# Performance work log

Measured on AMD Instinct MI355X. Metric: run time of the kernel, lower is better.

## Reference

```python
import jax, jax.numpy as jnp
import numpy as np

M, N, D, P = 16, 4096, 128, 8192
H = N // D


def setup_inputs() -> dict:
    key = jax.random.key(0)
    ks = jax.random.split(key, 6)
    return {
        "X": jax.random.normal(ks[0], (M, N), dtype=jnp.float32),
        "W_q": jax.random.normal(ks[1], (N, N), dtype=jnp.float32) / np.sqrt(N),
        "W_k": jax.random.normal(ks[2], (N, N), dtype=jnp.float32) / np.sqrt(N),
        "W_v": jax.random.normal(ks[3], (N, N), dtype=jnp.float32) / np.sqrt(N),
        "cache_K": jax.random.normal(ks[4], (H, P, D), dtype=jnp.float32),
        "cache_V": jax.random.normal(ks[5], (H, P, D), dtype=jnp.float32),
    }


def _rms(x):
    # unaffine RMS norm over last dim, no eps (matches torch source)
    return x * jax.lax.rsqrt(jnp.mean(jnp.square(x), axis=-1, keepdims=True))


def reference(X, W_q, W_k, W_v, cache_K, cache_V):
    m, n = X.shape
    h, p, d = cache_K.shape
    # QKV projections -> [H, M, D]
    q = (X @ W_q).reshape(m, h, d).swapaxes(0, 1)
    k = (X @ W_k).reshape(m, h, d).swapaxes(0, 1)
    v = (X @ W_v).reshape(m, h, d).swapaxes(0, 1)
    q_norm = _rms(q)
    k_norm = _rms(k)
    # prepend KV cache: [H, P+M, D]
    k_cache = jnp.concatenate([cache_K[:, :p, :], k_norm], axis=1)
    v_cache = jnp.concatenate([cache_V[:, :p, :], v], axis=1)
    # attention WITHOUT 1/sqrt(D) scaling (matches torch source)
    scores = jnp.einsum("hmd,hpd->hmp", q_norm, k_cache)
    weights = jax.nn.softmax(scores, axis=-1)
    out = jnp.einsum("hmp,hpd->hmd", weights, v_cache)  # [H, M, D]
    return out.swapaxes(0, 1).reshape(m, n)
```

## Files before the change

kernel.cpp:

```cpp
#include <hip/hip_runtime.h>
#include <math.h>

#define M_ 16
#define N_ 4096
#define D_ 128
#define P_ 8192
#define H_ 32

#define NIC 32
#define ICH (N_/NIC)
#define NCB 16

#define CHUNK 128
#define NCH (P_/CHUNK)
#define NCH1 (NCH+1)

#define QKV_SZ    (3*H_*M_*D_)
#define PART_OFF  (QKV_SZ)
#define OPART_OFF (QKV_SZ)
#define OPART_SZ  (H_*NCH1*M_*D_)
#define ML_OFF    (OPART_OFF + OPART_SZ)

__global__ __launch_bounds__(256) void k_proj(const float* __restrict__ X,
                                              const float* __restrict__ Wq,
                                              const float* __restrict__ Wk,
                                              const float* __restrict__ Wv,
                                              float* __restrict__ part) {
  const int mat = blockIdx.z;
  const float* __restrict__ W = (mat == 0) ? Wq : ((mat == 1) ? Wk : Wv);
  const int cb = blockIdx.x, ic = blockIdx.y;
  const int t = threadIdx.x;
  const int j0 = cb * 256 + t;
  const int i0 = ic * ICH;

  __shared__ __align__(16) float XT[ICH][20];

  {
    const int i_l = t & 127, mh = t >> 7;
#pragma unroll
    for (int r = 0; r < 8; ++r)
      XT[i_l][mh * 8 + r] = X[(size_t)(mh * 8 + r) * N_ + i0 + i_l];
  }
  __syncthreads();

  float acc[16];
#pragma unroll
  for (int m = 0; m < 16; ++m) acc[m] = 0.f;

#pragma unroll 8
  for (int i = 0; i < ICH; ++i) {
    const float wv = __builtin_nontemporal_load(W + (size_t)(i0 + i) * N_ + j0);
    float xr[16];
    {
      float4 xv;
      xv = *reinterpret_cast<const float4*>(&XT[i][0]);
      xr[0] = xv.x; xr[1] = xv.y; xr[2] = xv.z; xr[3] = xv.w;
      xv = *reinterpret_cast<const float4*>(&XT[i][4]);
      xr[4] = xv.x; xr[5] = xv.y; xr[6] = xv.z; xr[7] = xv.w;
      xv = *reinterpret_cast<const float4*>(&XT[i][8]);
      xr[8] = xv.x; xr[9] = xv.y; xr[10] = xv.z; xr[11] = xv.w;
      xv = *reinterpret_cast<const float4*>(&XT[i][12]);
      xr[12] = xv.x; xr[13] = xv.y; xr[14] = xv.z; xr[15] = xv.w;
    }
#pragma unroll
    for (int m = 0; m < 16; ++m) acc[m] = fmaf(xr[m], wv, acc[m]);
  }

#pragma unroll
  for (int m = 0; m < 16; ++m)
    __builtin_nontemporal_store(acc[m], part + (size_t)((mat * NIC + ic) * M_ + m) * N_ + j0);
}

__global__ __launch_bounds__(256) void k_reduce(const float* __restrict__ part,
                                                float* __restrict__ qkv) {
  const int mat = blockIdx.z, m = blockIdx.y, nc = blockIdx.x;
  const int t = threadIdx.x;
  const int n = nc * 256 + t;

  float s = 0.f;
#pragma unroll
  for (int ic = 0; ic < NIC; ++ic)
    s += __builtin_nontemporal_load(part + (size_t)((mat * NIC + ic) * M_ + m) * N_ + n);

  float ss = s * s;
#pragma unroll
  for (int off = 1; off < 64; off <<= 1) ss += __shfl_xor(ss, off);
  __shared__ float wsum[4];
  const int wave = t >> 6, lane = t & 63;
  if (lane == 0) wsum[wave] = ss;
  __syncthreads();
  const int half = t >> 7;
  const float tot = wsum[half * 2] + wsum[half * 2 + 1];
  const float scale = (mat < 2) ? rsqrtf(tot * (1.0f / 128.0f)) : 1.0f;

  const int h = n >> 7, d = n & 127;
  qkv[(size_t)((mat * H_ + h) * M_ + m) * D_ + d] = s * scale;
}

__device__ __forceinline__ float fold8(float a[8], int dq) {
#pragma unroll
  for (int i = 0; i < 4; ++i) {
    const float send = (dq & 4) ? a[i] : a[i + 4];
    const float recv = __shfl_xor(send, 4);
    a[i] = ((dq & 4) ? a[i + 4] : a[i]) + recv;
  }
#pragma unroll
  for (int i = 0; i < 2; ++i) {
    const float send = (dq & 2) ? a[i] : a[i + 2];
    const float recv = __shfl_xor(send, 2);
    a[i] = ((dq & 2) ? a[i + 2] : a[i]) + recv;
  }
  {
    const float send = (dq & 1) ? a[0] : a[1];
    const float recv = __shfl_xor(send, 1);
    a[0] = ((dq & 1) ? a[1] : a[0]) + recv;
  }
  return a[0];
}

__device__ __forceinline__ float dot16(const float* __restrict__ qrow,
                                       const float4 k0, const float4 k1,
                                       const float4 k2, const float4 k3) {
  const float4 q0 = *reinterpret_cast<const float4*>(qrow);
  const float4 q1 = *reinterpret_cast<const float4*>(qrow + 32);
  const float4 q2 = *reinterpret_cast<const float4*>(qrow + 64);
  const float4 q3 = *reinterpret_cast<const float4*>(qrow + 96);
  float s;
  s = q0.x * k0.x;
  s = fmaf(q0.y, k0.y, s); s = fmaf(q0.z, k0.z, s); s = fmaf(q0.w, k0.w, s);
  s = fmaf(q1.x, k1.x, s); s = fmaf(q1.y, k1.y, s);
  s = fmaf(q1.z, k1.z, s); s = fmaf(q1.w, k1.w, s);
  s = fmaf(q2.x, k2.x, s); s = fmaf(q2.y, k2.y, s);
  s = fmaf(q2.z, k2.z, s); s = fmaf(q2.w, k2.w, s);
  s = fmaf(q3.x, k3.x, s); s = fmaf(q3.y, k3.y, s);
  s = fmaf(q3.z, k3.z, s); s = fmaf(q3.w, k3.w, s);
  return s;
}

__global__ __launch_bounds__(512, 2) void k_attn(const float* __restrict__ cacheK,
                                                 const float* __restrict__ cacheV,
                                                 const float* __restrict__ qkv,
                                                 float* __restrict__ opart,
                                                 float* __restrict__ ml) {
  const int c = blockIdx.x, h = blockIdx.y;
  const int t = threadIdx.x;
  const int wave = t >> 6, lane = t & 63;
  const int valid = (c < NCH) ? CHUNK : M_;
  const float* __restrict__ Ksrc = (c < NCH)
      ? (cacheK + ((size_t)h * P_ + (size_t)c * CHUNK) * D_)
      : (qkv + (size_t)((1 * H_ + h) * M_) * D_);
  const float* __restrict__ Vsrc = (c < NCH)
      ? (cacheV + ((size_t)h * P_ + (size_t)c * CHUNK) * D_)
      : (qkv + (size_t)((2 * H_ + h) * M_) * D_);

  __shared__ __align__(16) float smem[8192];
  __shared__ __align__(16) float mlx[8][8][2];

  float* qs = smem;
  float* wxp = smem + 2048 + wave * 128;

  {
    const float4* src = reinterpret_cast<const float4*>(qkv + (size_t)(h * M_) * D_);
    reinterpret_cast<float4*>(qs)[t] = src[t];
  }
  __syncthreads();

  const int pg = lane >> 3, dq = lane & 7;
  const int dl = lane * 2;
  const int rg = wave >> 1, mbase = (wave & 1) * 8;
  const int rbase = rg * 32;
  int rc = valid - rbase; rc = (rc < 0) ? 0 : ((rc > 32) ? 32 : rc);
  const int nb = rc >> 4;

  float mrun = -3.0e38f, lrun = 0.f;
  float2 o[8];
#pragma unroll
  for (int mi = 0; mi < 8; ++mi) o[mi] = make_float2(0.f, 0.f);

#pragma unroll 1
  for (int b = 0; b < nb; ++b) {
    const int r0 = rbase + b * 16;

    float4 kA0, kA1, kA2, kA3, kB0, kB1, kB2, kB3;
    {
      const float* ka = Ksrc + (size_t)(r0 + pg) * D_ + dq * 4;
      kA0 = *reinterpret_cast<const float4*>(ka);
      kA1 = *reinterpret_cast<const float4*>(ka + 32);
      kA2 = *reinterpret_cast<const float4*>(ka + 64);
      kA3 = *reinterpret_cast<const float4*>(ka + 96);
      const float* kb = Ksrc + (size_t)(r0 + 8 + pg) * D_ + dq * 4;
      kB0 = *reinterpret_cast<const float4*>(kb);
      kB1 = *reinterpret_cast<const float4*>(kb + 32);
      kB2 = *reinterpret_cast<const float4*>(kb + 64);
      kB3 = *reinterpret_cast<const float4*>(kb + 96);
    }

    float a[8];
#pragma unroll
    for (int mi = 0; mi < 8; ++mi) {
      a[mi] = dot16(qs + (mbase + mi) * D_ + dq * 4, kA0, kA1, kA2, kA3);
      __builtin_amdgcn_sched_barrier(0);
    }
    const float sA = fold8(a, dq);

#pragma unroll
    for (int mi = 0; mi < 8; ++mi) {
      a[mi] = dot16(qs + (mbase + mi) * D_ + dq * 4, kB0, kB1, kB2, kB3);
      __builtin_amdgcn_sched_barrier(0);
    }
    const float sB = fold8(a, dq);

    float tmax = fmaxf(sA, sB);
    tmax = fmaxf(tmax, __shfl_xor(tmax, 8));
    tmax = fmaxf(tmax, __shfl_xor(tmax, 16));
    tmax = fmaxf(tmax, __shfl_xor(tmax, 32));
    const float mnew = fmaxf(mrun, tmax);
    const float fc = __expf(mrun - mnew);
    mrun = mnew;
    const float wA = __expf(sA - mnew);
    const float wB = __expf(sB - mnew);
    float rs = wA + wB;
    rs += __shfl_xor(rs, 8); rs += __shfl_xor(rs, 16); rs += __shfl_xor(rs, 32);
    lrun = lrun * fc + rs;

    wxp[pg * 8 + dq] = wA;
    wxp[(8 + pg) * 8 + dq] = wB;

#pragma unroll
    for (int mi = 0; mi < 8; ++mi) {
      const float fcm = __shfl(fc, (lane & 56) | mi);
      o[mi].x *= fcm; o[mi].y *= fcm;
    }

    float2 vvA[8], vvB[8];
#pragma unroll
    for (int j = 0; j < 8; ++j)
      vvA[j] = *reinterpret_cast<const float2*>(Vsrc + (size_t)(r0 + j) * D_ + dl);
#pragma unroll
    for (int j = 0; j < 8; ++j)
      vvB[j] = *reinterpret_cast<const float2*>(Vsrc + (size_t)(r0 + 8 + j) * D_ + dl);

#pragma unroll
    for (int j = 0; j < 8; ++j) {
      const float4 w0 = *reinterpret_cast<const float4*>(&wxp[j * 8]);
      const float4 w1 = *reinterpret_cast<const float4*>(&wxp[j * 8 + 4]);
      const float2 v = vvA[j];
#define PVM(i, wc) o[i].x = fmaf(wc, v.x, o[i].x); o[i].y = fmaf(wc, v.y, o[i].y);
      PVM(0, w0.x) PVM(1, w0.y) PVM(2, w0.z) PVM(3, w0.w)
      PVM(4, w1.x) PVM(5, w1.y) PVM(6, w1.z) PVM(7, w1.w)
#undef PVM
      if (j & 1) __builtin_amdgcn_sched_barrier(0);
    }
#pragma unroll
    for (int j = 0; j < 8; ++j) {
      const float4 w0 = *reinterpret_cast<const float4*>(&wxp[(8 + j) * 8]);
      const float4 w1 = *reinterpret_cast<const float4*>(&wxp[(8 + j) * 8 + 4]);
      const float2 v = vvB[j];
#define PVM(i, wc) o[i].x = fmaf(wc, v.x, o[i].x); o[i].y = fmaf(wc, v.y, o[i].y);
      PVM(0, w0.x) PVM(1, w0.y) PVM(2, w0.z) PVM(3, w0.w)
      PVM(4, w1.x) PVM(5, w1.y) PVM(6, w1.z) PVM(7, w1.w)
#undef PVM
      if (j & 1) __builtin_amdgcn_sched_barrier(0);
    }
  }

  __syncthreads();
  float* obuf = smem;
#pragma unroll
  for (int mi = 0; mi < 8; ++mi)
    *reinterpret_cast<float2*>(&obuf[wave * 1024 + mi * 128 + dl]) = o[mi];
  if (lane < 8) { mlx[wave][lane][0] = mrun; mlx[wave][lane][1] = lrun; }
  __syncthreads();

  {
    const int mm = t >> 5, seg = t & 31;
    const int w0i = mm >> 3, mi = mm & 7;
    float mv[4], lv[4];
#pragma unroll
    for (int r = 0; r < 4; ++r) { mv[r] = mlx[r * 2 + w0i][mi][0]; lv[r] = mlx[r * 2 + w0i][mi][1]; }
    const float mstar = fmaxf(fmaxf(mv[0], mv[1]), fmaxf(mv[2], mv[3]));
    float ew[4];
    float T = 0.f;
#pragma unroll
    for (int r = 0; r < 4; ++r) { ew[r] = __expf(mv[r] - mstar); T = fmaf(lv[r], ew[r], T); }
    float4 acc = make_float4(0.f, 0.f, 0.f, 0.f);
#pragma unroll
    for (int r = 0; r < 4; ++r) {
      const float4 v = *reinterpret_cast<const float4*>(&obuf[(r * 2 + w0i) * 1024 + mi * 128 + seg * 4]);
      acc.x = fmaf(ew[r], v.x, acc.x); acc.y = fmaf(ew[r], v.y, acc.y);
      acc.z = fmaf(ew[r], v.z, acc.z); acc.w = fmaf(ew[r], v.w, acc.w);
    }
    const size_t base = (size_t)((h * NCH1 + c) * M_ + mm) * D_;
    *reinterpret_cast<float4*>(opart + base + seg * 4) = acc;
    if (seg == 0) {
      ml[((size_t)(h * NCH1 + c) * M_ + mm) * 2 + 0] = mstar;
      ml[((size_t)(h * NCH1 + c) * M_ + mm) * 2 + 1] = T;
    }
  }
}

__global__ __launch_bounds__(128) void k_comb(const float* __restrict__ opart,
                                              const float* __restrict__ ml,
                                              float* __restrict__ out) {
  const int m = blockIdx.x, h = blockIdx.y, t = threadIdx.x;
  __shared__ float Ms[NCH1], Ls[NCH1];
  if (t < NCH1) {
    Ms[t] = ml[((size_t)(h * NCH1 + t) * M_ + m) * 2 + 0];
    Ls[t] = ml[((size_t)(h * NCH1 + t) * M_ + m) * 2 + 1];
  }
  __syncthreads();
  float gM = -3.0e38f;
#pragma unroll
  for (int c2 = 0; c2 < NCH1; ++c2) gM = fmaxf(gM, Ms[c2]);

  const float* __restrict__ ob = opart + (size_t)h * NCH1 * M_ * D_ + (size_t)m * D_ + t;
  float T = 0.f, o0 = 0.f, o1 = 0.f, o2 = 0.f, o3 = 0.f;
#pragma unroll 4
  for (int c2 = 0; c2 < NCH1 - 1; c2 += 4) {
    const float f0 = __expf(Ms[c2 + 0] - gM);
    const float f1 = __expf(Ms[c2 + 1] - gM);
    const float f2 = __expf(Ms[c2 + 2] - gM);
    const float f3 = __expf(Ms[c2 + 3] - gM);
    T = fmaf(Ls[c2 + 0], f0, T); T = fmaf(Ls[c2 + 1], f1, T);
    T = fmaf(Ls[c2 + 2], f2, T); T = fmaf(Ls[c2 + 3], f3, T);
    o0 = fmaf(ob[(size_t)(c2 + 0) * M_ * D_], f0, o0);
    o1 = fmaf(ob[(size_t)(c2 + 1) * M_ * D_], f1, o1);
    o2 = fmaf(ob[(size_t)(c2 + 2) * M_ * D_], f2, o2);
    o3 = fmaf(ob[(size_t)(c2 + 3) * M_ * D_], f3, o3);
  }
  {
    const int c2 = NCH1 - 1;
    const float f = __expf(Ms[c2] - gM);
    T = fmaf(Ls[c2], f, T);
    o0 = fmaf(ob[(size_t)c2 * M_ * D_], f, o0);
  }
  out[(size_t)m * N_ + h * D_ + t] = (o0 + o1 + o2 + o3) / T;
}

extern "C" void kernel_launch(void* const* d_in, const int* in_sizes, int n_in,
                              void* d_out, int out_size, void* d_ws, size_t ws_size,
                              hipStream_t stream) {
  const float* X  = (const float*)d_in[0];
  const float* Wq = (const float*)d_in[1];
  const float* Wk = (const float*)d_in[2];
  const float* Wv = (const float*)d_in[3];
  const float* cK = (const float*)d_in[4];
  const float* cV = (const float*)d_in[5];
  float* ws    = (float*)d_ws;
  float* qkv   = ws;
  float* part  = ws + PART_OFF;
  float* opart = ws + OPART_OFF;
  float* mlbuf = ws + ML_OFF;
  float* out   = (float*)d_out;

  hipLaunchKernelGGL(k_proj,   dim3(NCB, NIC, 3), dim3(256), 0, stream, X, Wq, Wk, Wv, part);
  hipLaunchKernelGGL(k_reduce, dim3(16, M_, 3),   dim3(256), 0, stream, part, qkv);
  hipLaunchKernelGGL(k_attn,   dim3(NCH1, H_),    dim3(512), 0, stream, cK, cV, qkv, opart, mlbuf);
  hipLaunchKernelGGL(k_comb,   dim3(M_, H_),      dim3(128), 0, stream, opart, mlbuf, out);
}
```

Before: 135.9 us.

## Prefetch next K tile into registers and issue V loads earlier in attention loop

K rows for the next 16-row block are loaded into registers during the current iteration (software pipelining), with indices clamped to stay in bounds. V loads are hoisted before the softmax reduction, and both QK dot products share each Q row read from shared memory. This is meant to hide global-memory latency behind compute and halve LDS reads of Q. It raises register pressure under launch_bounds(512,2), which risks spills, and adds one redundant K load per wave at the end.

```diff
diff --git a/kernel.cpp b/kernel.cpp
--- a/kernel.cpp
+++ b/kernel.cpp
@@ -116,25 +116,6 @@
     a[0] = ((dq & 1) ? a[1] : a[0]) + recv;
   }
   return a[0];
-}
-
-__device__ __forceinline__ float dot16(const float* __restrict__ qrow,
-                                       const float4 k0, const float4 k1,
-                                       const float4 k2, const float4 k3) {
-  const float4 q0 = *reinterpret_cast<const float4*>(qrow);
-  const float4 q1 = *reinterpret_cast<const float4*>(qrow + 32);
-  const float4 q2 = *reinterpret_cast<const float4*>(qrow + 64);
-  const float4 q3 = *reinterpret_cast<const float4*>(qrow + 96);
-  float s;
-  s = q0.x * k0.x;
-  s = fmaf(q0.y, k0.y, s); s = fmaf(q0.z, k0.z, s); s = fmaf(q0.w, k0.w, s);
-  s = fmaf(q1.x, k1.x, s); s = fmaf(q1.y, k1.y, s);
-  s = fmaf(q1.z, k1.z, s); s = fmaf(q1.w, k1.w, s);
-  s = fmaf(q2.x, k2.x, s); s = fmaf(q2.y, k2.y, s);
-  s = fmaf(q2.z, k2.z, s); s = fmaf(q2.w, k2.w, s);
-  s = fmaf(q3.x, k3.x, s); s = fmaf(q3.y, k3.y, s);
-  s = fmaf(q3.z, k3.z, s); s = fmaf(q3.w, k3.w, s);
-  return s;
 }
 
 __global__ __launch_bounds__(512, 2) void k_attn(const float* __restrict__ cacheK,
@@ -177,39 +158,80 @@
 #pragma unroll
   for (int mi = 0; mi < 8; ++mi) o[mi] = make_float2(0.f, 0.f);
 
+  float4 kk[8];
+  if (nb > 0) {
+    const float* ka = Ksrc + (size_t)(rbase + pg) * D_ + dq * 4;
+    kk[0] = *reinterpret_cast<const float4*>(ka);
+    kk[1] = *reinterpret_cast<const float4*>(ka + 32);
+    kk[2] = *reinterpret_cast<const float4*>(ka + 64);
+    kk[3] = *reinterpret_cast<const float4*>(ka + 96);
+    const float* kb = Ksrc + (size_t)(rbase + 8 + pg) * D_ + dq * 4;
+    kk[4] = *reinterpret_cast<const float4*>(kb);
+    kk[5] = *reinterpret_cast<const float4*>(kb + 32);
+    kk[6] = *reinterpret_cast<const float4*>(kb + 64);
+    kk[7] = *reinterpret_cast<const float4*>(kb + 96);
+  }
+
 #pragma unroll 1
   for (int b = 0; b < nb; ++b) {
     const int r0 = rbase + b * 16;
 
-    float4 kA0, kA1, kA2, kA3, kB0, kB1, kB2, kB3;
+    float aA[8], aB[8];
+#pragma unroll
+    for (int mi = 0; mi < 8; ++mi) {
+      const float* qrow = qs + (mbase + mi) * D_ + dq * 4;
+      const float4 q0 = *reinterpret_cast<const float4*>(qrow);
+      const float4 q1 = *reinterpret_cast<const float4*>(qrow + 32);
+      const float4 q2 = *reinterpret_cast<const float4*>(qrow + 64);
+      const float4 q3 = *reinterpret_cast<const float4*>(qrow + 96);
+      float sa, sb;
+      sa = q0.x * kk[0].x;
+      sa = fmaf(q0.y, kk[0].y, sa); sa = fmaf(q0.z, kk[0].z, sa); sa = fmaf(q0.w, kk[0].w, sa);
+      sa = fmaf(q1.x, kk[1].x, sa); sa = fmaf(q1.y, kk[1].y, sa);
+      sa = fmaf(q1.z, kk[1].z, sa); sa = fmaf(q1.w, kk[1].w, sa);
+      sa = fmaf(q2.x, kk[2].x, sa); sa = fmaf(q2.y, kk[2].y, sa);
+      sa = fmaf(q2.z, kk[2].z, sa); sa = fmaf(q2.w, kk[2].w, sa);
+      sa = fmaf(q3.x, kk[3].x, sa); sa = fmaf(q3.y, kk[3].y, sa);
+      sa = fmaf(q3.z, kk[3].z, sa); sa = fmaf(q3.w, kk[3].w, sa);
+      sb = q0.x * kk[4].x;
+      sb = fmaf(q0.y, kk[4].y, sb); sb = fmaf(q0.z, kk[4].z, sb); sb = fmaf(q0.w, kk[4].w, sb);
+      sb = fmaf(q1.x, kk[5].x, sb); sb = fmaf(q1.y, kk[5].y, sb);
+      sb = fmaf(q1.z, kk[5].z, sb); sb = fmaf(q1.w, kk[5].w, sb);
+      sb = fmaf(q2.x, kk[6].x, sb); sb = fmaf(q2.y, kk[6].y, sb);
+      sb = fmaf(q2.z, kk[6].z, sb); sb = fmaf(q2.w, kk[6].w, sb);
+      sb = fmaf(q3.x, kk[7].x, sb); sb = fmaf(q3.y, kk[7].y, sb);
+      sb = fmaf(q3.z, kk[7].z, sb); sb = fmaf(q3.w, kk[7].w, sb);
+      aA[mi] = sa; aB[mi] = sb;
+      __builtin_amdgcn_sched_barrier(0);
+    }
+
+    float2 vvA[8], vvB[8];
+#pragma unroll
+    for (int j = 0; j < 8; ++j)
+      vvA[j] = *reinterpret_cast<const float2*>(Vsrc + (size_t)(r0 + j) * D_ + dl);
+#pragma unroll
+    for (int j = 0; j < 8; ++j)
+      vvB[j] = *reinterpret_cast<const float2*>(Vsrc + (size_t)(r0 + 8 + j) * D_ + dl);
+
     {
-      const float* ka = Ksrc + (size_t)(r0 + pg) * D_ + dq * 4;
-      kA0 = *reinterpret_cast<const float4*>(ka);
-      kA1 = *reinterpret_cast<const float4*>(ka + 32);
-      kA2 = *reinterpret_cast<const float4*>(ka + 64);
-      kA3 = *reinterpret_cast<const float4*>(ka + 96);
-      const float* kb = Ksrc + (size_t)(r0 + 8 + pg) * D_ + dq * 4;
-      kB0 = *reinterpret_cast<const float4*>(kb);
-      kB1 = *reinterpret_cast<const float4*>(kb + 32);
-      kB2 = *reinterpret_cast<const float4*>(kb + 64);
-      kB3 = *reinterpret_cast<const float4*>(kb + 96);
-    }
-
-    float a[8];
-#pragma unroll
-    for (int mi = 0; mi < 8; ++mi) {
-      a[mi] = dot16(qs + (mbase + mi) * D_ + dq * 4, kA0, kA1, kA2, kA3);
-      __builtin_amdgcn_sched_barrier(0);
-    }
-    const float sA = fold8(a, dq);
-
-#pragma unroll
-    for (int mi = 0; mi < 8; ++mi) {
-      a[mi] = dot16(qs + (mbase + mi) * D_ + dq * 4, kB0, kB1, kB2, kB3);
-      __builtin_amdgcn_sched_barrier(0);
-    }
-    const float sB = fold8(a, dq);
-
+      int rn = r0 + 16 + pg;
+      rn = (rn < valid) ? rn : (valid - 1);
+      const float* ka = Ksrc + (size_t)rn * D_ + dq * 4;
+      kk[0] = *reinterpret_cast<const float4*>(ka);
+      kk[1] = *reinterpret_cast<const float4*>(ka + 32);
+      kk[2] = *reinterpret_cast<const float4*>(ka + 64);
+      kk[3] = *reinterpret_cast<const float4*>(ka + 96);
+      int rn2 = r0 + 24 + pg;
+      rn2 = (rn2 < valid) ? rn2 : (valid - 1);
+      const float* kb = Ksrc + (size_t)rn2 * D_ + dq * 4;
+      kk[4] = *reinterpret_cast<const float4*>(kb);
+      kk[5] = *reinterpret_cast<const float4*>(kb + 32);
+      kk[6] = *reinterpret_cast<const float4*>(kb + 64);
+      kk[7] = *reinterpret_cast<const float4*>(kb + 96);
+    }
+
+    const float sA = fold8(aA, dq);
+    const float sB = fold8(aB, dq);
     float tmax = fmaxf(sA, sB);
     tmax = fmaxf(tmax, __shfl_xor(tmax, 8));
     tmax = fmaxf(tmax, __shfl_xor(tmax, 16));
@@ -231,14 +253,6 @@
       const float fcm = __shfl(fc, (lane & 56) | mi);
       o[mi].x *= fcm; o[mi].y *= fcm;
     }
-
-    float2 vvA[8], vvB[8];
-#pragma unroll
-    for (int j = 0; j < 8; ++j)
-      vvA[j] = *reinterpret_cast<const float2*>(Vsrc + (size_t)(r0 + j) * D_ + dl);
-#pragma unroll
-    for (int j = 0; j < 8; ++j)
-      vvB[j] = *reinterpret_cast<const float2*>(Vsrc + (size_t)(r0 + 8 + j) * D_ + dl);
 
 #pragma unroll
     for (int j = 0; j < 8; ++j) {
```

Result: slower. 144.6 us (+6.4%).
